# Kernel tuning notes

Hardware: AMD Instinct MI355X
Metric: run time of the kernel (lower is better)

The kernel has to match this reference:

```python
import jax, jax.numpy as jnp
import numpy as np
from jax import lax

N_FFT = 16
HOP = 4
WIN_LEN = 16
OUT_WINDOW = 128  # adaptive pool output size
B, L, C = 32, 4096, 64
OUT_FEATURE = 512


def _stft_mag(x_bcl):
    # x_bcl: [B, C, L] float32. Replicates torch.stft(center=True, reflect pad,
    # periodic hann window, onesided) followed by abs().
    win = 0.5 * (1.0 - jnp.cos(2.0 * jnp.pi * jnp.arange(WIN_LEN) / WIN_LEN))  # periodic hann
    pad = N_FFT // 2
    xp = jnp.pad(x_bcl, ((0, 0), (0, 0), (pad, pad)), mode='reflect')
    T = 1 + x_bcl.shape[-1] // HOP  # centered frame count
    idx = np.arange(T)[:, None] * HOP + np.arange(N_FFT)[None, :]  # [T, n_fft] static
    frames = xp[..., idx]                       # [B, C, T, n_fft]
    spec = jnp.fft.rfft(frames * win, axis=-1)  # [B, C, T, F], F = n_fft//2+1
    return jnp.abs(spec).transpose(0, 1, 3, 2)  # [B, C, F, T]


def _adaptive_avg_pool1d(x_nct, out_size):
    # Matches torch adaptive_avg_pool1d: bin i covers [floor(i*N/out), ceil((i+1)*N/out))
    N = x_nct.shape[-1]
    starts = (np.arange(out_size) * N) // out_size
    ends = -((-(np.arange(out_size) + 1) * N) // out_size)  # ceil div
    csum = jnp.concatenate(
        [jnp.zeros(x_nct.shape[:-1] + (1,), x_nct.dtype), jnp.cumsum(x_nct, axis=-1)], axis=-1)
    sums = csum[..., ends] - csum[..., starts]
    counts = jnp.asarray(ends - starts, x_nct.dtype)
    return sums / counts


def setup_inputs() -> dict:
    key = jax.random.key(0)
    k1, k2, k3 = jax.random.split(key, 3)
    in_ch = C * (N_FFT // 2 + 1)  # 576
    x = jax.random.normal(k1, (B, L, C), dtype=jnp.float32)
    fan_in = in_ch * 3
    bound = 1.0 / np.sqrt(fan_in)
    weight = jax.random.uniform(k2, (OUT_FEATURE, in_ch, 3), jnp.float32, -bound, bound)
    bias = jax.random.uniform(k3, (OUT_FEATURE,), jnp.float32, -bound, bound)
    return {"x": x, "weight": weight, "bias": bias}


def reference(x, weight, bias):
    # x: [B, L, C]
    mags = _stft_mag(x.transpose(0, 2, 1))            # [B, C, F, T]
    Bb, Cc, F, T = mags.shape
    m = mags.reshape(Bb, Cc * F, T)                    # [B, C*F, T]
    y = lax.conv_general_dilated(
        m, weight, window_strides=(1,), padding='VALID',
        dimension_numbers=('NCH', 'OIH', 'NCH'))       # [B, out_feature, T-2]
    y = y + bias[None, :, None]
    y = _adaptive_avg_pool1d(y, OUT_WINDOW)            # [B, out_feature, window]
    return y.transpose(0, 2, 1)                        # [B, window, out_feature]
```

## Files before the change

### kernel.cpp

```cpp
#include <hip/hip_runtime.h>
#include <hip/hip_bf16.h>

#define BATCH 32
#define LTOT 4096
#define CCH 64
#define NFFT 16
#define HOP 4
#define NF 9
#define T_FR 1025
#define ICH 576
#define OCH 512
#define TY 1023
#define OUTW 128
#define KTOT 1728

typedef __attribute__((ext_vector_type(8))) _Float16 half8;
typedef __attribute__((ext_vector_type(4))) float floatx4;

__device__ constexpr float C16[16] = {
    1.0f,  0.923879533f,  0.707106781f,  0.382683432f,  0.0f, -0.382683432f,
   -0.707106781f, -0.923879533f, -1.0f, -0.923879533f, -0.707106781f,
   -0.382683432f,  0.0f,  0.382683432f,  0.707106781f,  0.923879533f};

#define C1F 0.923879533f
#define C2F 0.707106781f
#define C3F 0.382683432f

__device__ __forceinline__ void async_copy16(const _Float16* g, _Float16* l) {
  __builtin_amdgcn_global_load_lds(
      (const __attribute__((address_space(1))) unsigned int*)g,
      (__attribute__((address_space(3))) unsigned int*)l, 16, 0, 0);
}

__device__ __forceinline__ float fsqrt_fast(float v) {
  float r;
  asm("v_sqrt_f32 %0, %1" : "=v"(r) : "v"(v));
  return r;
}

#define SBAR() asm volatile("s_barrier" ::: "memory")
#define WAITV(N) asm volatile("s_waitcnt vmcnt(" #N ")" ::: "memory")

__global__ __launch_bounds__(256) void stft_pool_kernel(
    const float* __restrict__ x, const float* __restrict__ weight,
    _Float16* __restrict__ pm, _Float16* __restrict__ wkr) {
  const int w = blockIdx.x, b = blockIdx.y;
  const int tid = threadIdx.x;

  const int gid = (b * 128 + w) * 256 + tid;
  if (gid < OCH * ICH) {
    int o = gid / ICH, i = gid - o * ICH;
    int c = i / 9, f = i - c * 9;
    const float* src = weight + (size_t)o * (ICH * 3) + i * 3;
    _Float16* dst = wkr + (size_t)o * KTOT + f * 64 + c;
#pragma unroll
    for (int k = 0; k < 3; ++k)
      dst[k * ICH] = (_Float16)src[k];
  }

  const int s = (w * TY) >> 7;
  const int e = ((w + 1) * TY + 127) >> 7;
  const int cnt = e - s;
  const int R = cnt + 2;
  const float inv = 1.0f / (float)cnt;

  __shared__ float arena[56 * 64];
  float* xs = arena;
  float* red = arena;

  const int l_base = s * 4 - 8;
  const int nrow = R * 4 + 12;
  const float* xb = x + (size_t)b * LTOT * CCH;
#pragma unroll
  for (int it = 0; it < 4; ++it) {
    int u = it * 256 + tid;
    int r = u >> 4, c4 = u & 15;
    if (r < nrow) {
      int l = l_base + r;
      if (l < 0) l = -l;
      if (l >= LTOT) l = 2 * LTOT - 2 - l;
      *(floatx4*)(&xs[r * 64 + c4 * 4]) =
          *(const floatx4*)(&xb[(size_t)l * CCH + c4 * 4]);
    }
  }
  __syncthreads();

  const int c = tid & 63, tq = tid >> 6;

  float acc[3][NF];
#pragma unroll
  for (int k = 0; k < 3; ++k)
#pragma unroll
    for (int f = 0; f < NF; ++f) acc[k][f] = 0.0f;

#pragma unroll
  for (int it = 0; it < 3; ++it) {
    const int rl = tq + it * 4;
    if (rl < R) {
      float wx[16];
#pragma unroll
      for (int j = 0; j < 16; ++j)
        wx[j] = xs[(rl * 4 + j) * 64 + c] * (0.5f * (1.0f - C16[j]));
      const float s1 = wx[1] + wx[15], d1 = wx[1] - wx[15];
      const float s2 = wx[2] + wx[14], d2 = wx[2] - wx[14];
      const float s3 = wx[3] + wx[13], d3 = wx[3] - wx[13];
      const float s4 = wx[4] + wx[12], d4 = wx[4] - wx[12];
      const float s5 = wx[5] + wx[11], d5 = wx[5] - wx[11];
      const float s6 = wx[6] + wx[10], d6 = wx[6] - wx[10];
      const float s7 = wx[7] + wx[9],  d7 = wx[7] - wx[9];
      const float wxp = wx[0] + wx[8], wxm = wx[0] - wx[8];
      const float u1 = s2 - s6, u2 = s1 - s7, u3 = s3 - s5;
      const float v1 = d2 + d6, v2 = d1 + d7, v3 = d3 + d5;
      const float Se = s2 + s4 + s6;
      const float So = (s1 + s3) + (s5 + s7);
      const float re0 = wxp + Se + So;
      const float re8 = wxp + (Se - So);
      const float tA = C2F * u1;
      const float A1 = wxm + tA, A3 = wxm - tA;
      const float B1 = C1F * u2 + C3F * u3;
      const float B3 = C3F * u2 - C1F * u3;
      const float tP = C2F * v1;
      const float P1 = d4 + tP, P3 = tP - d4;
      const float Q1 = C3F * v2 + C1F * v3;
      const float Q3 = C1F * v2 - C3F * v3;
      const float A2 = wxp - s4;
      const float B2 = C2F * (((s1 - s3) - s5) + s7);
      const float P2 = d2 - d6;
      const float Q2 = C2F * (((d1 + d3) - d5) - d7);
      const float re4 = ((wxp - s2) + s4) - s6;
      const float im4 = ((d1 - d3) + d5) - d7;

      float mg[NF];
      mg[0] = fabsf(re0);
      mg[8] = fabsf(re8);
      {
        const float r1 = A1 + B1, i1 = P1 + Q1;
        mg[1] = fsqrt_fast(r1 * r1 + i1 * i1);
        const float r7 = A1 - B1, i7 = Q1 - P1;
        mg[7] = fsqrt_fast(r7 * r7 + i7 * i7);
        const float r2 = A2 + B2, i2 = P2 + Q2;
        mg[2] = fsqrt_fast(r2 * r2 + i2 * i2);
        const float r6 = A2 - B2, i6 = Q2 - P2;
        mg[6] = fsqrt_fast(r6 * r6 + i6 * i6);
        const float r3 = A3 + B3, i3 = P3 + Q3;
        mg[3] = fsqrt_fast(r3 * r3 + i3 * i3);
        const float r5 = A3 - B3, i5 = Q3 - P3;
        mg[5] = fsqrt_fast(r5 * r5 + i5 * i5);
        mg[4] = fsqrt_fast(re4 * re4 + im4 * im4);
      }
#pragma unroll
      for (int k = 0; k < 3; ++k)
        if ((unsigned)(rl - k) < (unsigned)cnt)
#pragma unroll
          for (int f = 0; f < NF; ++f) acc[k][f] += mg[f];
    }
  }

  __syncthreads();

  if (tq < 2) {
#pragma unroll
    for (int k = 0; k < 3; ++k)
#pragma unroll
      for (int f = 0; f < NF; ++f)
        red[((tq * 27) + k * 9 + f) * 64 + c] = acc[k][f];
  }
  __syncthreads();
  if (tq >= 2) {
#pragma unroll
    for (int k = 0; k < 3; ++k)
#pragma unroll
      for (int f = 0; f < NF; ++f) {
        const int idx = (((tq - 2) * 27) + k * 9 + f) * 64 + c;
        red[idx] += acc[k][f];
      }
  }
  __syncthreads();

  _Float16* pmo = pm + ((size_t)b * OUTW + w) * KTOT;
  for (int j = tid; j < KTOT; j += 256) {
    const int k = j / ICH;
    const int rem = j - k * ICH;
    const int f = rem >> 6;
    const int cc = rem & 63;
    const int base = (k * 9 + f) * 64 + cc;
    const float sum = red[base] + red[27 * 64 + base];
    pmo[j] = (_Float16)(sum * inv);
  }
}

__global__ __launch_bounds__(256, 2) void gemm_pooled_kernel(
    const _Float16* __restrict__ pm, const _Float16* __restrict__ wkr,
    const float* __restrict__ bias, float* __restrict__ out) {
  const int lid = blockIdx.x;
  const int xcd = lid & 7;
  const int rest = lid >> 3;
  const int m8 = rest & 7;
  const int bq = rest >> 3;
  const int b = bq * 8 + xcd;
  const int o0 = m8 * 64;

  const int tid = threadIdx.x;
  const int wave = tid >> 6, lane = tid & 63;
  const int wm = wave >> 1, wn = wave & 1;

  __shared__ _Float16 as[2][64 * 64];
  __shared__ _Float16 bs[2][128 * 64];

  floatx4 acc[2][4];
#pragma unroll
  for (int mt = 0; mt < 2; ++mt)
#pragma unroll
    for (int nt = 0; nt < 4; ++nt)
      acc[mt][nt] = (floatx4)0.0f;

  const int frow = lane & 15;
  const int quad = lane >> 4;
  const int l7 = lane & 7;
  const int srow = lane >> 3;
  const int ssrc_off = srow * KTOT + (l7 ^ srow) * 8;

  const _Float16* ab = wkr + (size_t)o0 * KTOT;
  const _Float16* bb = pm + (size_t)b * OUTW * KTOT;

#define GSTAGE(kbx, buf)                                                     \
  {                                                                          \
    const int i0s = (kbx) * 64;                                              \
    _Pragma("unroll") for (int it = 0; it < 2; ++it) {                       \
      const int seg = wave * 2 + it;                                         \
      async_copy16(ab + (size_t)(seg * 8) * KTOT + i0s + ssrc_off,           \
                   &as[buf][seg * 512]);                                     \
    }                                                                        \
    _Pragma("unroll") for (int it = 0; it < 4; ++it) {                       \
      const int seg = wave * 4 + it;                                         \
      async_copy16(bb + (size_t)(seg * 8) * KTOT + i0s + ssrc_off,           \
                   &bs[buf][seg * 512]);                                     \
    }                                                                        \
  }

  GSTAGE(0, 0);
  for (int kb = 0; kb < 27; ++kb) {
    const int cur = kb & 1;
    if (kb < 26) {
      GSTAGE(kb + 1, cur ^ 1);
      WAITV(6);
    } else {
      WAITV(0);
    }
    SBAR();

#pragma unroll
    for (int kk2 = 0; kk2 < 2; ++kk2) {
      const int jj = kk2 * 4 + quad;
      const int coff = ((jj ^ l7) << 3);
      half8 af[2], bf[4];
#pragma unroll
      for (int mt = 0; mt < 2; ++mt)
        af[mt] =
            *(const half8*)(&as[cur][(wm * 32 + mt * 16 + frow) * 64 + coff]);
#pragma unroll
      for (int nt = 0; nt < 4; ++nt)
        bf[nt] =
            *(const half8*)(&bs[cur][(wn * 64 + nt * 16 + frow) * 64 + coff]);
#pragma unroll
      for (int mt = 0; mt < 2; ++mt)
#pragma unroll
        for (int nt = 0; nt < 4; ++nt)
          acc[mt][nt] = __builtin_amdgcn_mfma_f32_16x16x32_f16(
              bf[nt], af[mt], acc[mt][nt], 0, 0, 0);
    }
    SBAR();
  }

  const int col = lane & 15;
  float* ob = out + (size_t)b * OUTW * OCH;
#pragma unroll
  for (int nt = 0; nt < 4; ++nt) {
    const int wb = wn * 64 + nt * 16 + quad * 4;
#pragma unroll
    for (int r = 0; r < 4; ++r) {
      const int w = wb + r;
#pragma unroll
      for (int mt = 0; mt < 2; ++mt) {
        const int o = o0 + wm * 32 + mt * 16 + col;
        ob[(size_t)w * OCH + o] = bias[o] + acc[mt][nt][r];
      }
    }
  }
}

extern "C" void kernel_launch(void* const* d_in, const int* in_sizes, int n_in,
                              void* d_out, int out_size, void* d_ws, size_t ws_size,
                              hipStream_t stream) {
  const float* x = (const float*)d_in[0];
  const float* weight = (const float*)d_in[1];
  const float* bias = (const float*)d_in[2];
  float* out = (float*)d_out;

  char* ws = (char*)d_ws;
  const size_t w_bytes = (size_t)OCH * KTOT * sizeof(_Float16);
  _Float16* wkr = (_Float16*)ws;
  _Float16* pm = (_Float16*)(ws + w_bytes);

  hipLaunchKernelGGL(stft_pool_kernel, dim3(OUTW, BATCH), dim3(256), 0,
                     stream, x, weight, pm, wkr);
  hipLaunchKernelGGL(gemm_pooled_kernel, dim3(256), dim3(256), 0, stream,
                     pm, wkr, bias, out);
}
```

Measured before the change: 112.6 us.

## Split STFT pooling into per-frame magnitude kernel and windowed mean kernel

The fused STFT plus pooling kernel is split in two. The first kernel computes each frame's magnitudes exactly once and writes them in fp16 to a workspace. A second kernel averages the shifted frame windows into the pooled GEMM operand. Before, overlapping pooling windows recomputed the FFT for the frames at their edges. The cost is an extra launch and a round trip of about 38 MB through global memory, plus fp16 rounding of the intermediate magnitudes before averaging.

```diff
diff --git a/kernel.cpp b/kernel.cpp
--- a/kernel.cpp
+++ b/kernel.cpp
@@ -8,6 +8,7 @@
 #define HOP 4
 #define NF 9
 #define T_FR 1025
+#define T_ROWS 1032
 #define ICH 576
 #define OCH 512
 #define TY 1023
@@ -41,13 +42,14 @@
 #define SBAR() asm volatile("s_barrier" ::: "memory")
 #define WAITV(N) asm volatile("s_waitcnt vmcnt(" #N ")" ::: "memory")
 
-__global__ __launch_bounds__(256) void stft_pool_kernel(
+__global__ __launch_bounds__(256) void stft_wrepack_kernel(
     const float* __restrict__ x, const float* __restrict__ weight,
-    _Float16* __restrict__ pm, _Float16* __restrict__ wkr) {
-  const int w = blockIdx.x, b = blockIdx.y;
+    _Float16* __restrict__ m_ws, _Float16* __restrict__ wkr) {
+  const int b = blockIdx.y;
+  const int t0 = blockIdx.x * 4;
   const int tid = threadIdx.x;
 
-  const int gid = (b * 128 + w) * 256 + tid;
+  const int gid = (b * 258 + blockIdx.x) * 256 + tid;
   if (gid < OCH * ICH) {
     int o = gid / ICH, i = gid - o * ICH;
     int c = i / 9, f = i - c * 9;
@@ -58,25 +60,15 @@
       dst[k * ICH] = (_Float16)src[k];
   }
 
-  const int s = (w * TY) >> 7;
-  const int e = ((w + 1) * TY + 127) >> 7;
-  const int cnt = e - s;
-  const int R = cnt + 2;
-  const float inv = 1.0f / (float)cnt;
-
-  __shared__ float arena[56 * 64];
-  float* xs = arena;
-  float* red = arena;
-
-  const int l_base = s * 4 - 8;
-  const int nrow = R * 4 + 12;
+  __shared__ float xs[28 * 64];
+  const int l0 = t0 * HOP - 8;
   const float* xb = x + (size_t)b * LTOT * CCH;
 #pragma unroll
-  for (int it = 0; it < 4; ++it) {
-    int u = it * 256 + tid;
-    int r = u >> 4, c4 = u & 15;
-    if (r < nrow) {
-      int l = l_base + r;
+  for (int it = 0; it < 2; ++it) {
+    int e = it * 256 + tid;
+    int r = e >> 4, c4 = e & 15;
+    if (r < 28) {
+      int l = l0 + r;
       if (l < 0) l = -l;
       if (l >= LTOT) l = 2 * LTOT - 2 - l;
       *(floatx4*)(&xs[r * 64 + c4 * 4]) =
@@ -86,107 +78,91 @@
   __syncthreads();
 
   const int c = tid & 63, tq = tid >> 6;
-
-  float acc[3][NF];
-#pragma unroll
-  for (int k = 0; k < 3; ++k)
-#pragma unroll
-    for (int f = 0; f < NF; ++f) acc[k][f] = 0.0f;
-
-#pragma unroll
-  for (int it = 0; it < 3; ++it) {
-    const int rl = tq + it * 4;
-    if (rl < R) {
-      float wx[16];
-#pragma unroll
-      for (int j = 0; j < 16; ++j)
-        wx[j] = xs[(rl * 4 + j) * 64 + c] * (0.5f * (1.0f - C16[j]));
-      const float s1 = wx[1] + wx[15], d1 = wx[1] - wx[15];
-      const float s2 = wx[2] + wx[14], d2 = wx[2] - wx[14];
-      const float s3 = wx[3] + wx[13], d3 = wx[3] - wx[13];
-      const float s4 = wx[4] + wx[12], d4 = wx[4] - wx[12];
-      const float s5 = wx[5] + wx[11], d5 = wx[5] - wx[11];
-      const float s6 = wx[6] + wx[10], d6 = wx[6] - wx[10];
-      const float s7 = wx[7] + wx[9],  d7 = wx[7] - wx[9];
-      const float wxp = wx[0] + wx[8], wxm = wx[0] - wx[8];
-      const float u1 = s2 - s6, u2 = s1 - s7, u3 = s3 - s5;
-      const float v1 = d2 + d6, v2 = d1 + d7, v3 = d3 + d5;
-      const float Se = s2 + s4 + s6;
-      const float So = (s1 + s3) + (s5 + s7);
-      const float re0 = wxp + Se + So;
-      const float re8 = wxp + (Se - So);
-      const float tA = C2F * u1;
-      const float A1 = wxm + tA, A3 = wxm - tA;
-      const float B1 = C1F * u2 + C3F * u3;
-      const float B3 = C3F * u2 - C1F * u3;
-      const float tP = C2F * v1;
-      const float P1 = d4 + tP, P3 = tP - d4;
-      const float Q1 = C3F * v2 + C1F * v3;
-      const float Q3 = C1F * v2 - C3F * v3;
-      const float A2 = wxp - s4;
-      const float B2 = C2F * (((s1 - s3) - s5) + s7);
-      const float P2 = d2 - d6;
-      const float Q2 = C2F * (((d1 + d3) - d5) - d7);
-      const float re4 = ((wxp - s2) + s4) - s6;
-      const float im4 = ((d1 - d3) + d5) - d7;
-
-      float mg[NF];
-      mg[0] = fabsf(re0);
-      mg[8] = fabsf(re8);
-      {
-        const float r1 = A1 + B1, i1 = P1 + Q1;
-        mg[1] = fsqrt_fast(r1 * r1 + i1 * i1);
-        const float r7 = A1 - B1, i7 = Q1 - P1;
-        mg[7] = fsqrt_fast(r7 * r7 + i7 * i7);
-        const float r2 = A2 + B2, i2 = P2 + Q2;
-        mg[2] = fsqrt_fast(r2 * r2 + i2 * i2);
-        const float r6 = A2 - B2, i6 = Q2 - P2;
-        mg[6] = fsqrt_fast(r6 * r6 + i6 * i6);
-        const float r3 = A3 + B3, i3 = P3 + Q3;
-        mg[3] = fsqrt_fast(r3 * r3 + i3 * i3);
-        const float r5 = A3 - B3, i5 = Q3 - P3;
-        mg[5] = fsqrt_fast(r5 * r5 + i5 * i5);
-        mg[4] = fsqrt_fast(re4 * re4 + im4 * im4);
-      }
-#pragma unroll
-      for (int k = 0; k < 3; ++k)
-        if ((unsigned)(rl - k) < (unsigned)cnt)
-#pragma unroll
-          for (int f = 0; f < NF; ++f) acc[k][f] += mg[f];
-    }
-  }
-
-  __syncthreads();
-
-  if (tq < 2) {
-#pragma unroll
-    for (int k = 0; k < 3; ++k)
-#pragma unroll
-      for (int f = 0; f < NF; ++f)
-        red[((tq * 27) + k * 9 + f) * 64 + c] = acc[k][f];
-  }
-  __syncthreads();
-  if (tq >= 2) {
-#pragma unroll
-    for (int k = 0; k < 3; ++k)
-#pragma unroll
-      for (int f = 0; f < NF; ++f) {
-        const int idx = (((tq - 2) * 27) + k * 9 + f) * 64 + c;
-        red[idx] += acc[k][f];
-      }
-  }
-  __syncthreads();
-
-  _Float16* pmo = pm + ((size_t)b * OUTW + w) * KTOT;
-  for (int j = tid; j < KTOT; j += 256) {
-    const int k = j / ICH;
-    const int rem = j - k * ICH;
-    const int f = rem >> 6;
-    const int cc = rem & 63;
-    const int base = (k * 9 + f) * 64 + cc;
-    const float sum = red[base] + red[27 * 64 + base];
-    pmo[j] = (_Float16)(sum * inv);
-  }
+  const int t = t0 + tq;
+  _Float16* o_ptr = m_ws + ((size_t)b * T_ROWS + t) * ICH + c;
+  if (t >= T_FR) {
+#pragma unroll
+    for (int f = 0; f < NF; ++f) o_ptr[f * 64] = (_Float16)0.0f;
+    return;
+  }
+
+  float wx[16];
+#pragma unroll
+  for (int j = 0; j < 16; ++j)
+    wx[j] = xs[(tq * 4 + j) * 64 + c] * (0.5f * (1.0f - C16[j]));
+  const float s1 = wx[1] + wx[15], d1 = wx[1] - wx[15];
+  const float s2 = wx[2] + wx[14], d2 = wx[2] - wx[14];
+  const float s3 = wx[3] + wx[13], d3 = wx[3] - wx[13];
+  const float s4 = wx[4] + wx[12], d4 = wx[4] - wx[12];
+  const float s5 = wx[5] + wx[11], d5 = wx[5] - wx[11];
+  const float s6 = wx[6] + wx[10], d6 = wx[6] - wx[10];
+  const float s7 = wx[7] + wx[9],  d7 = wx[7] - wx[9];
+  const float wxp = wx[0] + wx[8], wxm = wx[0] - wx[8];
+  const float u1 = s2 - s6, u2 = s1 - s7, u3 = s3 - s5;
+  const float v1 = d2 + d6, v2 = d1 + d7, v3 = d3 + d5;
+  const float Se = s2 + s4 + s6;
+  const float So = (s1 + s3) + (s5 + s7);
+  const float re0 = wxp + Se + So;
+  const float re8 = wxp + (Se - So);
+  const float tA = C2F * u1;
+  const float A1 = wxm + tA, A3 = wxm - tA;
+  const float B1 = C1F * u2 + C3F * u3;
+  const float B3 = C3F * u2 - C1F * u3;
+  const float tP = C2F * v1;
+  const float P1 = d4 + tP, P3 = tP - d4;
+  const float Q1 = C3F * v2 + C1F * v3;
+  const float Q3 = C1F * v2 - C3F * v3;
+  const float A2 = wxp - s4;
+  const float B2 = C2F * (((s1 - s3) - s5) + s7);
+  const float P2 = d2 - d6;
+  const float Q2 = C2F * (((d1 + d3) - d5) - d7);
+  const float re4 = ((wxp - s2) + s4) - s6;
+  const float im4 = ((d1 - d3) + d5) - d7;
+
+  o_ptr[0 * 64] = (_Float16)fabsf(re0);
+  o_ptr[8 * 64] = (_Float16)fabsf(re8);
+  {
+    const float r1 = A1 + B1, i1 = P1 + Q1;
+    o_ptr[1 * 64] = (_Float16)fsqrt_fast(r1 * r1 + i1 * i1);
+    const float r7 = A1 - B1, i7 = Q1 - P1;
+    o_ptr[7 * 64] = (_Float16)fsqrt_fast(r7 * r7 + i7 * i7);
+    const float r2 = A2 + B2, i2 = P2 + Q2;
+    o_ptr[2 * 64] = (_Float16)fsqrt_fast(r2 * r2 + i2 * i2);
+    const float r6 = A2 - B2, i6 = Q2 - P2;
+    o_ptr[6 * 64] = (_Float16)fsqrt_fast(r6 * r6 + i6 * i6);
+    const float r3 = A3 + B3, i3 = P3 + Q3;
+    o_ptr[3 * 64] = (_Float16)fsqrt_fast(r3 * r3 + i3 * i3);
+    const float r5 = A3 - B3, i5 = Q3 - P3;
+    o_ptr[5 * 64] = (_Float16)fsqrt_fast(r5 * r5 + i5 * i5);
+    o_ptr[4 * 64] = (_Float16)fsqrt_fast(re4 * re4 + im4 * im4);
+  }
+}
+
+__global__ __launch_bounds__(256) void pmean_kernel(
+    const _Float16* __restrict__ m_ws, _Float16* __restrict__ pm) {
+  const int w = blockIdx.x, b = blockIdx.y;
+  const int j = threadIdx.x;
+  if (j >= 216) return;
+  const int k = j / 72;
+  const int i8 = (j - k * 72) * 8;
+  const int s = (w * TY) >> 7;
+  const int e = ((w + 1) * TY + 127) >> 7;
+  const int cnt = e - s;
+  const float inv = 1.0f / (float)cnt;
+  const _Float16* src =
+      m_ws + ((size_t)b * T_ROWS + s + k) * ICH + i8;
+  float acc[8];
+#pragma unroll
+  for (int q = 0; q < 8; ++q) acc[q] = 0.0f;
+  for (int t = 0; t < cnt; ++t) {
+    half8 v = *(const half8*)(src + (size_t)t * ICH);
+#pragma unroll
+    for (int q = 0; q < 8; ++q) acc[q] += (float)v[q];
+  }
+  half8 r;
+#pragma unroll
+  for (int q = 0; q < 8; ++q) r[q] = (_Float16)(acc[q] * inv);
+  *(half8*)(pm + ((size_t)(b * OUTW + w)) * KTOT + j * 8) = r;
 }
 
 __global__ __launch_bounds__(256, 2) void gemm_pooled_kernel(
@@ -299,11 +275,15 @@
 
   char* ws = (char*)d_ws;
   const size_t w_bytes = (size_t)OCH * KTOT * sizeof(_Float16);
+  const size_t m_bytes = (size_t)BATCH * T_ROWS * ICH * sizeof(_Float16);
   _Float16* wkr = (_Float16*)ws;
-  _Float16* pm = (_Float16*)(ws + w_bytes);
-
-  hipLaunchKernelGGL(stft_pool_kernel, dim3(OUTW, BATCH), dim3(256), 0,
-                     stream, x, weight, pm, wkr);
+  _Float16* m_ws = (_Float16*)(ws + w_bytes);
+  _Float16* pm = (_Float16*)(ws + w_bytes + m_bytes);
+
+  hipLaunchKernelGGL(stft_wrepack_kernel, dim3(258, BATCH), dim3(256), 0,
+                     stream, x, weight, m_ws, wkr);
+  hipLaunchKernelGGL(pmean_kernel, dim3(OUTW, BATCH), dim3(256), 0, stream,
+                     m_ws, pm);
   hipLaunchKernelGGL(gemm_pooled_kernel, dim3(256), dim3(256), 0, stream,
                      pm, wkr, bias, out);
 }
```

Measured after the change: 119.3 us. 1.06x slower.

## Assign one pooling window per wave, four windows per block, drop LDS reduction

Applied to the files above, without the earlier changes.

The STFT/pool kernel now has each block cover four consecutive output windows, with each wave computing one whole window serially instead of four waves splitting one window. Overlapping input rows are loaded into shared memory once per block. The cross-wave shared-memory reduction and its barriers are removed, and results are written directly from registers. The grid shrinks from 128 to 32 blocks per batch and the weight reorder becomes a grid-stride loop, which lowers parallelism and lengthens each thread's serial frame loop.

```diff
diff --git a/kernel.cpp b/kernel.cpp
--- a/kernel.cpp
+++ b/kernel.cpp
@@ -44,149 +44,120 @@
 __global__ __launch_bounds__(256) void stft_pool_kernel(
     const float* __restrict__ x, const float* __restrict__ weight,
     _Float16* __restrict__ pm, _Float16* __restrict__ wkr) {
-  const int w = blockIdx.x, b = blockIdx.y;
+  const int wg = blockIdx.x;
+  const int b = blockIdx.y;
   const int tid = threadIdx.x;
 
-  const int gid = (b * 128 + w) * 256 + tid;
-  if (gid < OCH * ICH) {
+  for (int gid = (b * 32 + wg) * 256 + tid; gid < OCH * ICH;
+       gid += 32 * BATCH * 256) {
     int o = gid / ICH, i = gid - o * ICH;
-    int c = i / 9, f = i - c * 9;
+    int cc = i / 9, f = i - cc * 9;
     const float* src = weight + (size_t)o * (ICH * 3) + i * 3;
-    _Float16* dst = wkr + (size_t)o * KTOT + f * 64 + c;
+    _Float16* dst = wkr + (size_t)o * KTOT + f * 64 + cc;
 #pragma unroll
     for (int k = 0; k < 3; ++k)
       dst[k * ICH] = (_Float16)src[k];
   }
 
+  const int w0 = wg * 4;
+  const int s0 = (w0 * TY) >> 7;
+  const int e3 = ((w0 + 4) * TY + 127) >> 7;
+  const int RM = e3 + 2 - s0;
+  const int nrow = RM * 4 + 12;
+
+  __shared__ float xs[152 * 64];
+
+  const int l0 = s0 * 4 - 8;
+  const float* xb = x + (size_t)b * LTOT * CCH;
+  for (int u = tid; u < nrow * 16; u += 256) {
+    int r = u >> 4, c4 = u & 15;
+    int l = l0 + r;
+    if (l < 0) l = -l;
+    if (l >= LTOT) l = 2 * LTOT - 2 - l;
+    *(floatx4*)(&xs[r * 64 + c4 * 4]) =
+        *(const floatx4*)(&xb[(size_t)l * CCH + c4 * 4]);
+  }
+  __syncthreads();
+
+  const int c = tid & 63, tq = tid >> 6;
+  const int w = w0 + tq;
   const int s = (w * TY) >> 7;
   const int e = ((w + 1) * TY + 127) >> 7;
   const int cnt = e - s;
-  const int R = cnt + 2;
   const float inv = 1.0f / (float)cnt;
 
-  __shared__ float arena[56 * 64];
-  float* xs = arena;
-  float* red = arena;
-
-  const int l_base = s * 4 - 8;
-  const int nrow = R * 4 + 12;
-  const float* xb = x + (size_t)b * LTOT * CCH;
-#pragma unroll
-  for (int it = 0; it < 4; ++it) {
-    int u = it * 256 + tid;
-    int r = u >> 4, c4 = u & 15;
-    if (r < nrow) {
-      int l = l_base + r;
-      if (l < 0) l = -l;
-      if (l >= LTOT) l = 2 * LTOT - 2 - l;
-      *(floatx4*)(&xs[r * 64 + c4 * 4]) =
-          *(const floatx4*)(&xb[(size_t)l * CCH + c4 * 4]);
-    }
-  }
-  __syncthreads();
-
-  const int c = tid & 63, tq = tid >> 6;
-
   float acc[3][NF];
 #pragma unroll
   for (int k = 0; k < 3; ++k)
 #pragma unroll
     for (int f = 0; f < NF; ++f) acc[k][f] = 0.0f;
 
-#pragma unroll
-  for (int it = 0; it < 3; ++it) {
-    const int rl = tq + it * 4;
-    if (rl < R) {
-      float wx[16];
-#pragma unroll
-      for (int j = 0; j < 16; ++j)
-        wx[j] = xs[(rl * 4 + j) * 64 + c] * (0.5f * (1.0f - C16[j]));
-      const float s1 = wx[1] + wx[15], d1 = wx[1] - wx[15];
-      const float s2 = wx[2] + wx[14], d2 = wx[2] - wx[14];
-      const float s3 = wx[3] + wx[13], d3 = wx[3] - wx[13];
-      const float s4 = wx[4] + wx[12], d4 = wx[4] - wx[12];
-      const float s5 = wx[5] + wx[11], d5 = wx[5] - wx[11];
-      const float s6 = wx[6] + wx[10], d6 = wx[6] - wx[10];
-      const float s7 = wx[7] + wx[9],  d7 = wx[7] - wx[9];
-      const float wxp = wx[0] + wx[8], wxm = wx[0] - wx[8];
-      const float u1 = s2 - s6, u2 = s1 - s7, u3 = s3 - s5;
-      const float v1 = d2 + d6, v2 = d1 + d7, v3 = d3 + d5;
-      const float Se = s2 + s4 + s6;
-      const float So = (s1 + s3) + (s5 + s7);
-      const float re0 = wxp + Se + So;
-      const float re8 = wxp + (Se - So);
-      const float tA = C2F * u1;
-      const float A1 = wxm + tA, A3 = wxm - tA;
-      const float B1 = C1F * u2 + C3F * u3;
-      const float B3 = C3F * u2 - C1F * u3;
-      const float tP = C2F * v1;
-      const float P1 = d4 + tP, P3 = tP - d4;
-      const float Q1 = C3F * v2 + C1F * v3;
-      const float Q3 = C1F * v2 - C3F * v3;
-      const float A2 = wxp - s4;
-      const float B2 = C2F * (((s1 - s3) - s5) + s7);
-      const float P2 = d2 - d6;
-      const float Q2 = C2F * (((d1 + d3) - d5) - d7);
-      const float re4 = ((wxp - s2) + s4) - s6;
-      const float im4 = ((d1 - d3) + d5) - d7;
-
-      float mg[NF];
-      mg[0] = fabsf(re0);
-      mg[8] = fabsf(re8);
-      {
-        const float r1 = A1 + B1, i1 = P1 + Q1;
-        mg[1] = fsqrt_fast(r1 * r1 + i1 * i1);
-        const float r7 = A1 - B1, i7 = Q1 - P1;
-        mg[7] = fsqrt_fast(r7 * r7 + i7 * i7);
-        const float r2 = A2 + B2, i2 = P2 + Q2;
-        mg[2] = fsqrt_fast(r2 * r2 + i2 * i2);
-        const float r6 = A2 - B2, i6 = Q2 - P2;
-        mg[6] = fsqrt_fast(r6 * r6 + i6 * i6);
-        const float r3 = A3 + B3, i3 = P3 + Q3;
-        mg[3] = fsqrt_fast(r3 * r3 + i3 * i3);
-        const float r5 = A3 - B3, i5 = Q3 - P3;
-        mg[5] = fsqrt_fast(r5 * r5 + i5 * i5);
-        mg[4] = fsqrt_fast(re4 * re4 + im4 * im4);
-      }
-#pragma unroll
-      for (int k = 0; k < 3; ++k)
-        if ((unsigned)(rl - k) < (unsigned)cnt)
-#pragma unroll
-          for (int f = 0; f < NF; ++f) acc[k][f] += mg[f];
-    }
-  }
-
-  __syncthreads();
-
-  if (tq < 2) {
+  for (int t = s; t <= e + 1; ++t) {
+    const int rb = (t - s0) * 4;
+    float wx[16];
+#pragma unroll
+    for (int j = 0; j < 16; ++j)
+      wx[j] = xs[(rb + j) * 64 + c] * (0.5f * (1.0f - C16[j]));
+    const float s1 = wx[1] + wx[15], d1 = wx[1] - wx[15];
+    const float s2 = wx[2] + wx[14], d2 = wx[2] - wx[14];
+    const float s3 = wx[3] + wx[13], d3 = wx[3] - wx[13];
+    const float s4 = wx[4] + wx[12], d4 = wx[4] - wx[12];
+    const float s5 = wx[5] + wx[11], d5 = wx[5] - wx[11];
+    const float s6 = wx[6] + wx[10], d6 = wx[6] - wx[10];
+    const float s7 = wx[7] + wx[9],  d7 = wx[7] - wx[9];
+    const float wxp = wx[0] + wx[8], wxm = wx[0] - wx[8];
+    const float u1 = s2 - s6, u2 = s1 - s7, u3 = s3 - s5;
+    const float v1 = d2 + d6, v2 = d1 + d7, v3 = d3 + d5;
+    const float Se = s2 + s4 + s6;
+    const float So = (s1 + s3) + (s5 + s7);
+    const float re0 = wxp + Se + So;
+    const float re8 = wxp + (Se - So);
+    const float tA = C2F * u1;
+    const float A1 = wxm + tA, A3 = wxm - tA;
+    const float B1 = C1F * u2 + C3F * u3;
+    const float B3 = C3F * u2 - C1F * u3;
+    const float tP = C2F * v1;
+    const float P1 = d4 + tP, P3 = tP - d4;
+    const float Q1 = C3F * v2 + C1F * v3;
+    const float Q3 = C1F * v2 - C3F * v3;
+    const float A2 = wxp - s4;
+    const float B2 = C2F * (((s1 - s3) - s5) + s7);
+    const float P2 = d2 - d6;
+    const float Q2 = C2F * (((d1 + d3) - d5) - d7);
+    const float re4 = ((wxp - s2) + s4) - s6;
+    const float im4 = ((d1 - d3) + d5) - d7;
+
+    float mg[NF];
+    mg[0] = fabsf(re0);
+    mg[8] = fabsf(re8);
+    {
+      const float r1 = A1 + B1, i1 = P1 + Q1;
+      mg[1] = fsqrt_fast(r1 * r1 + i1 * i1);
+      const float r7 = A1 - B1, i7 = Q1 - P1;
+      mg[7] = fsqrt_fast(r7 * r7 + i7 * i7);
+      const float r2 = A2 + B2, i2 = P2 + Q2;
+      mg[2] = fsqrt_fast(r2 * r2 + i2 * i2);
+      const float r6 = A2 - B2, i6 = Q2 - P2;
+      mg[6] = fsqrt_fast(r6 * r6 + i6 * i6);
+      const float r3 = A3 + B3, i3 = P3 + Q3;
+      mg[3] = fsqrt_fast(r3 * r3 + i3 * i3);
+      const float r5 = A3 - B3, i5 = Q3 - P3;
+      mg[5] = fsqrt_fast(r5 * r5 + i5 * i5);
+      mg[4] = fsqrt_fast(re4 * re4 + im4 * im4);
+    }
 #pragma unroll
     for (int k = 0; k < 3; ++k)
-#pragma unroll
-      for (int f = 0; f < NF; ++f)
-        red[((tq * 27) + k * 9 + f) * 64 + c] = acc[k][f];
-  }
-  __syncthreads();
-  if (tq >= 2) {
-#pragma unroll
-    for (int k = 0; k < 3; ++k)
-#pragma unroll
-      for (int f = 0; f < NF; ++f) {
-        const int idx = (((tq - 2) * 27) + k * 9 + f) * 64 + c;
-        red[idx] += acc[k][f];
-      }
-  }
-  __syncthreads();
+      if ((unsigned)(t - k - s) < (unsigned)cnt)
+#pragma unroll
+        for (int f = 0; f < NF; ++f) acc[k][f] += mg[f];
+  }
 
   _Float16* pmo = pm + ((size_t)b * OUTW + w) * KTOT;
-  for (int j = tid; j < KTOT; j += 256) {
-    const int k = j / ICH;
-    const int rem = j - k * ICH;
-    const int f = rem >> 6;
-    const int cc = rem & 63;
-    const int base = (k * 9 + f) * 64 + cc;
-    const float sum = red[base] + red[27 * 64 + base];
-    pmo[j] = (_Float16)(sum * inv);
-  }
+#pragma unroll
+  for (int k = 0; k < 3; ++k)
+#pragma unroll
+    for (int f = 0; f < NF; ++f)
+      pmo[k * ICH + f * 64 + c] = (_Float16)(acc[k][f] * inv);
 }
 
 __global__ __launch_bounds__(256, 2) void gemm_pooled_kernel(
@@ -302,7 +273,7 @@
   _Float16* wkr = (_Float16*)ws;
   _Float16* pm = (_Float16*)(ws + w_bytes);
 
-  hipLaunchKernelGGL(stft_pool_kernel, dim3(OUTW, BATCH), dim3(256), 0,
+  hipLaunchKernelGGL(stft_pool_kernel, dim3(32, BATCH), dim3(256), 0,
                      stream, x, weight, pm, wkr);
   hipLaunchKernelGGL(gemm_pooled_kernel, dim3(256), dim3(256), 0, stream,
                      pm, wkr, bias, out);
```

Result: no change. 114.6 us (+1.7%).
